# Kernel tuning notes

Measured on AMD Instinct MI355X. Metric: run time of the kernel, lower is better.

## Reference

```python
import jax, jax.numpy as jnp
import numpy as np

B, M, PAST, FUT, NPRED, D = 512, 32768, 8, 12, 20, 48


def _gru_step(h, x, w_ih, w_hh, b_ih, b_hh):
    # torch GRU cell: gates ordered [r, z, n]
    gi = x @ w_ih.T + b_ih
    gh = h @ w_hh.T + b_hh
    ir, iz, inn = jnp.split(gi, 3, axis=-1)
    hr, hz, hn = jnp.split(gh, 3, axis=-1)
    r = jax.nn.sigmoid(ir + hr)
    z = jax.nn.sigmoid(iz + hz)
    n = jnp.tanh(inn + r * hn)
    return (1.0 - z) * n + z * h


def setup_inputs() -> dict:
    key = jax.random.key(0)
    ks = jax.random.split(key, 16)
    f32 = jnp.float32
    def rn(k, shp, sc):
        return (jax.random.normal(k, shp, dtype=f32) * sc)
    return {
        "past": jax.random.normal(ks[0], (B, PAST, 2), dtype=f32),
        "obs_traj": jax.random.normal(ks[1], (B, PAST, 2), dtype=f32),
        "conv_w": rn(ks[2], (D, 2, 3), 0.3),
        "conv_b": jnp.zeros((D,), f32),
        "enc_w_ih": rn(ks[3], (3 * D, D), 0.1),
        "enc_w_hh": rn(ks[4], (3 * D, D), 0.1),
        "enc_b_ih": jnp.zeros((3 * D,), f32),
        "enc_b_hh": jnp.zeros((3 * D,), f32),
        "memory_past": jax.random.normal(ks[5], (M, D), dtype=f32),
        "memory_fut": jax.random.normal(ks[6], (M, D), dtype=f32),
        "Wq": rn(ks[7], (D, D), 0.1), "bq": jnp.zeros((D,), f32),
        "Wk": rn(ks[8], (D, D), 0.1), "bk": jnp.zeros((D,), f32),
        "Wv": rn(ks[9], (D, D), 0.1), "bv": jnp.zeros((D,), f32),
        "dec_w_ih": rn(ks[10], (6 * D, 2 * D), 0.1),
        "dec_w_hh": rn(ks[11], (6 * D, 2 * D), 0.1),
        "dec_b_ih": jnp.zeros((6 * D,), f32),
        "dec_b_hh": jnp.zeros((6 * D,), f32),
        "fc_w": rn(ks[12], (2, 2 * D), 0.1),
        "fc_b": jnp.zeros((2,), f32),
    }


def reference(past, obs_traj, conv_w, conv_b, enc_w_ih, enc_w_hh, enc_b_ih, enc_b_hh,
              memory_past, memory_fut, Wq, bq, Wk, bk, Wv, bv,
              dec_w_ih, dec_w_hh, dec_b_ih, dec_b_hh, fc_w, fc_b):
    b = past.shape[0]
    # --- past encoder: Conv1d(2,48,3,pad=1) + ReLU, then GRU(48,48) ---
    x = jnp.transpose(past, (0, 2, 1))                     # [B,2,T]
    emb = jax.lax.conv_general_dilated(
        x, conv_w, (1,), [(1, 1)], dimension_numbers=("NCH", "OIH", "NCH"))
    emb = jax.nn.relu(emb + conv_b[None, :, None])         # [B,48,T]
    emb = jnp.transpose(emb, (2, 0, 1))                    # [T,B,48] for scan

    def enc_step(h, x_t):
        return _gru_step(h, x_t, enc_w_ih, enc_w_hh, enc_b_ih, enc_b_hh), None
    state_past, _ = jax.lax.scan(enc_step, jnp.zeros((b, D), past.dtype), emb)  # [B,48]

    # --- iterative refinement: 20 rounds of attention over the full memory ---
    # Lin_K/Lin_V are applied to the same (full) banks every iteration -> hoist.
    K = memory_past @ Wk.T + bk                            # [M,48]
    V = memory_fut @ Wv.T + bv                             # [M,48]

    def irm_step(c, _):
        q = c @ Wq.T + bq                                  # [B,48]
        a = jax.nn.softmax(q @ K.T, axis=-1)               # [B,M], scale=1.0
        att = a @ V                                        # [B,48]
        return q + att, att
    _, atts = jax.lax.scan(irm_step, state_past, None, length=NPRED)  # [20,B,48]
    pred = jnp.transpose(atts, (1, 0, 2)).reshape(-1, D)   # [B*20,48] (b-major)

    # --- GRU(96,96) decoder, future_len steps, input only at t=0 ---
    n = b * NPRED
    present = jnp.repeat(obs_traj[:, -1], NPRED, axis=0)   # [B*20,2]
    sp = jnp.repeat(state_past, NPRED, axis=0)             # [B*20,48]
    info = jnp.concatenate([sp, pred], axis=1)             # [B*20,96]
    xs = jnp.concatenate(
        [info[None], jnp.zeros((FUT - 1, n, 2 * D), info.dtype)], axis=0)

    def dec_step(carry, x_t):
        h, pres = carry
        h = _gru_step(h, x_t, dec_w_ih, dec_w_hh, dec_b_ih, dec_b_hh)
        pres = pres + (h @ fc_w.T + fc_b)
        return (h, pres), pres
    _, coords = jax.lax.scan(
        dec_step, (jnp.zeros((n, 2 * D), info.dtype), present), xs)  # [FUT,B*20,2]

    prediction = jnp.transpose(coords, (1, 0, 2)).reshape(b, NPRED, FUT, 2)
    return prediction
```

## Files before the change

kernel.cpp:

```cpp
#include <hip/hip_runtime.h>

typedef unsigned short u16;
typedef unsigned int u32;
typedef __attribute__((ext_vector_type(8))) short short8v;
typedef __attribute__((ext_vector_type(4))) float f32x4;

#define GLD_LDS(g, l) __builtin_amdgcn_global_load_lds( \
    (const __attribute__((address_space(1))) void*)(g), \
    (__attribute__((address_space(3))) void*)(l), 16, 0, 0)

#define LOG2E 1.44269504f

__device__ __forceinline__ u16 f2bf(float f){
  union { float f; u32 u; } v; v.f = f;
  u32 r = v.u + 0x7FFFu + ((v.u >> 16) & 1u);
  return (u16)(r >> 16);
}
__device__ __forceinline__ float bf2f(u16 h){
  union { u32 u; float f; } v; v.u = ((u32)h) << 16;
  return v.f;
}
__device__ __forceinline__ u32 pk2(float a, float b){
  union { float f; u32 u; } x, y; x.f = a; y.f = b;
  return __builtin_amdgcn_perm(y.u + 0x8000u, x.u + 0x8000u, 0x07060302u);
}
__device__ __forceinline__ float sigm(float x){ return 1.f/(1.f+__expf(-x)); }
__device__ __forceinline__ float tanh_fast(float x){ return 1.f - 2.f/(1.f+__expf(2.f*x)); }

__global__ __launch_bounds__(256) void setup_kernel(
    const float* past, const float* conv_w, const float* conv_b,
    const float* enc_w_ih, const float* enc_w_hh, const float* enc_b_ih, const float* enc_b_hh,
    const float* memory_past, const float* memory_fut,
    const float* Wq, const float* bq, const float* Wk, const float* bk,
    const float* Wv, const float* bv,
    const float* dec_w_ih, const float* dec_w_hh,
    float* stateP, float* qf, u16* qbB,
    u16* Kb, u16* Vc, u16* Dihf, u16* Dhhf, u16* WqF)
{
  __shared__ __align__(16) char SMEM[61440];
  const int tid = threadIdx.x, bx = blockIdx.x;
  const int wid = tid>>6, lane = tid&63, qd = lane>>4, ln = lane&15;
  f32x4 zf = {0.f,0.f,0.f,0.f};

  if (tid < 108){
    int which = (tid >= 54) ? 1 : 0;
    int e = bx*54 + (tid - which*54);
    const float* src = which ? dec_w_hh : dec_w_ih;
    u16* dst = which ? Dhhf : Dihf;
    int j = e&7, l2 = (e>>3)&15, q2 = (e>>7)&3, tkc = e>>9;
    int kc = tkc % 3, nt = tkc / 3;
    dst[e] = f2bf(src[(nt*16+l2)*96 + kc*32 + q2*8 + j]);
  }
  if (bx < 12){
    int e = bx*256 + tid;
    int j = e&7, l2 = (e>>3)&15, q2 = (e>>7)&3, tkc = e>>9;
    int kc = tkc&1, nt = tkc>>1;
    int g = nt*16+l2, k = kc*32+q2*8+j;
    WqF[e] = (k < 48) ? f2bf(Wq[g*48+k]) : (u16)0;
  }

  if (bx >= 504){
    int eb = bx - 504;
    u16* sWih = (u16*)(SMEM);
    u16* sWhh = (u16*)(SMEM + 18432);
    u16* sWq  = (u16*)(SMEM + 36864);
    float* sCw = (float*)(SMEM + 43008);
    float* sCb = (float*)(SMEM + 44160);
    float* sPast = (float*)(SMEM + 44352);
    u16* sHbW = (u16*)(SMEM + 48448 + wid*2304);
    for (int e0 = tid; e0 < 21504; e0 += 256){
      int e = e0; const float* src; u16* dst;
      if (e < 9216){ src = enc_w_ih; dst = sWih; }
      else if (e < 18432){ e -= 9216; src = enc_w_hh; dst = sWhh; }
      else { e -= 18432; src = Wq; dst = sWq; }
      int j = e&7, l2 = (e>>3)&15, q2 = (e>>7)&3, tkc = e>>9;
      int kc = tkc&1, nt = tkc>>1;
      int g = nt*16+l2, k = kc*32+q2*8+j;
      dst[e] = (k < 48) ? f2bf(src[g*48+k]) : (u16)0;
    }
    for (int i = tid; i < 288; i += 256) sCw[i] = conv_w[i];
    if (tid < 48) sCb[tid] = conv_b[tid];
    for (int i = tid; i < 1024; i += 256) sPast[i] = past[eb*1024 + i];
    __syncthreads();
    short8v aE[8][2];
    {
      const float* pr = &sPast[(wid*16 + ln)*16];
      for (int t = 0; t < 8; ++t)
        for (int kc = 0; kc < 2; ++kc){
          union { short8v v; u16 h[8]; } u;
          #pragma unroll
          for (int j = 0; j < 8; ++j){
            int d = kc*32 + qd*8 + j;
            float a = 0.f;
            if (d < 48){
              a = sCb[d];
              #pragma unroll
              for (int kt = 0; kt < 3; ++kt){
                int tau = t + kt - 1;
                if (tau >= 0 && tau < 8){
                  a += pr[tau*2+0]*sCw[d*6+kt];
                  a += pr[tau*2+1]*sCw[d*6+3+kt];
                }
              }
              a = fmaxf(a, 0.f);
            }
            u.h[j] = (d < 48) ? f2bf(a) : (u16)0;
          }
          aE[t][kc] = u.v;
        }
    }
    for (int i = lane; i < 576; i += 64) ((u32*)sHbW)[i] = 0;
    float biR[3],biZ[3],biN[3],bhR[3],bhZ[3],bhN[3];
    #pragma unroll
    for (int i = 0; i < 3; ++i){
      int d = i*16 + ln;
      biR[i]=enc_b_ih[d]; biZ[i]=enc_b_ih[48+d]; biN[i]=enc_b_ih[96+d];
      bhR[i]=enc_b_hh[d]; bhZ[i]=enc_b_hh[48+d]; bhN[i]=enc_b_hh[96+d];
    }
    float hreg[3][4];
    #pragma unroll
    for (int i=0;i<3;++i) for (int r=0;r<4;++r) hreg[i][r]=0.f;
    int r0 = eb*64 + wid*16;
    #pragma unroll 1
    for (int t = 0; t < 8; ++t){
      short8v aH0 = *(const short8v*)&sHbW[ln*72 + qd*8];
      short8v aH1 = *(const short8v*)&sHbW[ln*72 + 32 + qd*8];
      f32x4 gI[9], gH[9];
      #pragma unroll
      for (int nt = 0; nt < 9; ++nt){ gI[nt] = zf; gH[nt] = zf; }
      #pragma unroll
      for (int nt = 0; nt < 9; ++nt){
        gI[nt] = __builtin_amdgcn_mfma_f32_16x16x32_bf16(aE[t][0], *(const short8v*)&sWih[((nt*2+0)*4+qd)*128 + ln*8], gI[nt], 0,0,0);
        gI[nt] = __builtin_amdgcn_mfma_f32_16x16x32_bf16(aE[t][1], *(const short8v*)&sWih[((nt*2+1)*4+qd)*128 + ln*8], gI[nt], 0,0,0);
        gH[nt] = __builtin_amdgcn_mfma_f32_16x16x32_bf16(aH0, *(const short8v*)&sWhh[((nt*2+0)*4+qd)*128 + ln*8], gH[nt], 0,0,0);
        gH[nt] = __builtin_amdgcn_mfma_f32_16x16x32_bf16(aH1, *(const short8v*)&sWhh[((nt*2+1)*4+qd)*128 + ln*8], gH[nt], 0,0,0);
      }
      #pragma unroll
      for (int i3 = 0; i3 < 3; ++i3)
        #pragma unroll
        for (int r = 0; r < 4; ++r){
          float rr = sigm(gI[i3][r]+biR[i3] + gH[i3][r]+bhR[i3]);
          float zz = sigm(gI[i3+3][r]+biZ[i3] + gH[i3+3][r]+bhZ[i3]);
          float nn = tanh_fast(gI[i3+6][r]+biN[i3] + rr*(gH[i3+6][r]+bhN[i3]));
          float hv = (1.f-zz)*nn + zz*hreg[i3][r];
          hreg[i3][r] = hv;
          sHbW[(qd*4+r)*72 + i3*16 + ln] = f2bf(hv);
        }
    }
    #pragma unroll
    for (int i3 = 0; i3 < 3; ++i3)
      #pragma unroll
      for (int r = 0; r < 4; ++r)
        stateP[(r0+qd*4+r)*48 + i3*16 + ln] = hreg[i3][r];
    short8v aH0 = *(const short8v*)&sHbW[ln*72 + qd*8];
    short8v aH1 = *(const short8v*)&sHbW[ln*72 + 32 + qd*8];
    f32x4 q3[3];
    #pragma unroll
    for (int nt = 0; nt < 3; ++nt){
      q3[nt] = zf;
      q3[nt] = __builtin_amdgcn_mfma_f32_16x16x32_bf16(aH0, *(const short8v*)&sWq[((nt*2+0)*4+qd)*128 + ln*8], q3[nt], 0,0,0);
      q3[nt] = __builtin_amdgcn_mfma_f32_16x16x32_bf16(aH1, *(const short8v*)&sWq[((nt*2+1)*4+qd)*128 + ln*8], q3[nt], 0,0,0);
    }
    #pragma unroll
    for (int nt = 0; nt < 3; ++nt)
      #pragma unroll
      for (int r = 0; r < 4; ++r){
        int row = r0 + qd*4 + r, d = nt*16 + ln;
        float v = q3[nt][r] + bq[d];
        qf[row*48 + d] = v;
        qbB[row*64 + d] = f2bf(v * LOG2E);
      }
    #pragma unroll
    for (int r = 0; r < 4; ++r)
      if (ln < 8) *(u32*)&qbB[(r0+qd*4+r)*64 + 48 + ln*2] = 0;
  } else {
    u16* sWkF = (u16*)(SMEM);
    u16* sWvF = (u16*)(SMEM + 6144);
    u16* smp  = (u16*)(SMEM + 12288 + wid*2304);
    u16* smf  = (u16*)(SMEM + 21504 + wid*2304);
    for (int e0 = tid; e0 < 6144; e0 += 256){
      int e = e0; const float* src; u16* dst;
      if (e < 3072){ src = Wk; dst = sWkF; } else { e -= 3072; src = Wv; dst = sWvF; }
      int j = e&7, l2 = (e>>3)&15, q2 = (e>>7)&3, tkc = e>>9;
      int kc = tkc&1, nt = tkc>>1;
      int g = nt*16+l2, k = kc*32+q2*8+j;
      dst[e] = (k < 48) ? f2bf(src[g*48+k]) : (u16)0;
    }
    __syncthreads();
    int ntile = (bx < 8) ? 2 : 1;
    for (int tt = 0; tt < ntile; ++tt){
      int tile = (tt == 0) ? bx : (504 + bx);
      int r0 = tile*64 + wid*16;
      for (int i = lane; i < 576; i += 64){ ((u32*)smp)[i] = 0; ((u32*)smf)[i] = 0; }
      for (int i = lane; i < 768; i += 64){
        int r = i/48, c = i - r*48;
        smp[r*72+c] = f2bf(memory_past[(size_t)r0*48 + i]);
        smf[r*72+c] = f2bf(memory_fut[(size_t)r0*48 + i]);
      }
      short8v aP0 = *(const short8v*)&smp[ln*72 + qd*8];
      short8v aP1 = *(const short8v*)&smp[ln*72 + 32 + qd*8];
      short8v aF0 = *(const short8v*)&smf[ln*72 + qd*8];
      short8v aF1 = *(const short8v*)&smf[ln*72 + 32 + qd*8];
      f32x4 k3[3], v3[3];
      #pragma unroll
      for (int nt = 0; nt < 3; ++nt){ k3[nt] = zf; v3[nt] = zf; }
      #pragma unroll
      for (int nt = 0; nt < 3; ++nt){
        k3[nt] = __builtin_amdgcn_mfma_f32_16x16x32_bf16(aP0, *(const short8v*)&sWkF[((nt*2+0)*4+qd)*128 + ln*8], k3[nt], 0,0,0);
        k3[nt] = __builtin_amdgcn_mfma_f32_16x16x32_bf16(aP1, *(const short8v*)&sWkF[((nt*2+1)*4+qd)*128 + ln*8], k3[nt], 0,0,0);
        v3[nt] = __builtin_amdgcn_mfma_f32_16x16x32_bf16(aF0, *(const short8v*)&sWvF[((nt*2+0)*4+qd)*128 + ln*8], v3[nt], 0,0,0);
        v3[nt] = __builtin_amdgcn_mfma_f32_16x16x32_bf16(aF1, *(const short8v*)&sWvF[((nt*2+1)*4+qd)*128 + ln*8], v3[nt], 0,0,0);
      }
      #pragma unroll
      for (int nt = 0; nt < 3; ++nt)
        #pragma unroll
        for (int r = 0; r < 4; ++r){
          int key = r0 + qd*4 + r, d = nt*16 + ln;
          Kb[(size_t)key*64 + d] = f2bf(k3[nt][r] + bk[d]);
          Vc[((size_t)(key>>8)*48 + d)*256 + (key&255)] = f2bf(v3[nt][r] + bv[d]);
        }
      #pragma unroll
      for (int r = 0; r < 4; ++r)
        if (ln < 8){ int key = r0 + qd*4 + r; *(u32*)&Kb[(size_t)key*64 + 48 + ln*2] = 0; }
    }
  }
}

__global__ __launch_bounds__(256) void iter_kernel(int mode, int it,
    const u16* qbB, const u16* Kb, const u16* Vc, const u16* WqF, const float* bq,
    const float* qfP, float* qfC, float* pred,
    const float* mP, const float* lP, const float* aP,
    float* mC, float* lC, float* aC)
{
  __shared__ __align__(16) char SMEM[55936];
  u16*   sQ  = (u16*)(SMEM + 45056);
  float* sWc = (float*)(SMEM + 49152);
  float* sLg = (float*)(SMEM + 51200);
  u16*   sCb = (u16*)(SMEM + 51332);
  const int tid = threadIdx.x, bx = blockIdx.x;
  const int wid = tid>>6, lane = tid&63, qd = lane>>4, ln = lane&15;
  const int rg = bx>>4, ch = bx&15;
  const int rowbase = rg*32;
  f32x4 zf = {0.f,0.f,0.f,0.f};

  const int wslice = ch*2048 + wid*512;
  short8v kf0[4][2], vf0[2][3];
  {
    const u16* kb = Kb + (size_t)wslice*64;
    const u16* vb = Vc + (size_t)(wslice>>8)*48*256 + (wslice & 255);
    #pragma unroll
    for (int nt = 0; nt < 4; ++nt)
      #pragma unroll
      for (int kc = 0; kc < 2; ++kc)
        kf0[nt][kc] = *(const short8v*)&kb[(nt*16+ln)*64 + kc*32 + qd*8];
    #pragma unroll
    for (int kc = 0; kc < 2; ++kc)
      #pragma unroll
      for (int dt = 0; dt < 3; ++dt)
        vf0[kc][dt] = *(const short8v*)&vb[(dt*16+ln)*256 + kc*32 + qd*8];
  }

  if (mode == 1){
    float* sRed = (float*)SMEM;
    {
      int row = tid>>3, jj = tid&7, grow = rowbase + row;
      float m0 = mP[grow*16 + jj*2], m1 = mP[grow*16 + jj*2+1];
      float l0 = lP[grow*16 + jj*2], l1 = lP[grow*16 + jj*2+1];
      float mg = fmaxf(m0, m1);
      #pragma unroll
      for (int k = 1; k < 8; k <<= 1) mg = fmaxf(mg, __shfl_xor(mg, k));
      float w0 = exp2f(m0 - mg), w1 = exp2f(m1 - mg);
      float wl = w0*l0 + w1*l1;
      #pragma unroll
      for (int k = 1; k < 8; k <<= 1) wl += __shfl_xor(wl, k);
      sWc[row*16 + jj*2] = w0; sWc[row*16 + jj*2+1] = w1;
      if (jj == 0) sLg[row] = wl;
    }
    __syncthreads();
    {
      f32x4 accv[6];
      #pragma unroll
      for (int i = 0; i < 6; ++i) accv[i] = zf;
      #pragma unroll
      for (int ci = 0; ci < 4; ++ci){
        int c = wid*4 + ci;
        const f32x4* slab = (const f32x4*)(aP + ((size_t)c*512 + rowbase)*48);
        #pragma unroll
        for (int i = 0; i < 6; ++i){
          f32x4 v = slab[i*64 + lane];
          int rr = (i*64 + lane)/12;
          float w = sWc[rr*16 + c];
          accv[i][0] += w*v[0]; accv[i][1] += w*v[1];
          accv[i][2] += w*v[2]; accv[i][3] += w*v[3];
        }
      }
      float* red = sRed + wid*1536;
      #pragma unroll
      for (int i = 0; i < 6; ++i)
        *(f32x4*)&red[(i*64 + lane)*4] = accv[i];
    }
    __syncthreads();
    {
      int row = tid>>3, jj = tid&7, grow = rowbase + row;
      float lg = sLg[row];
      int base = row*48 + jj*6;
      #pragma unroll
      for (int d6 = 0; d6 < 6; ++d6){
        int d = jj*6 + d6;
        float s = sRed[base+d6] + sRed[1536+base+d6] + sRed[3072+base+d6] + sRed[4608+base+d6];
        float a = s / lg;
        if (ch == 0) pred[(size_t)(grow*20 + (it-1))*48 + d] = a;
        sCb[row*72 + d] = f2bf(qfP[grow*48 + d] + a);
      }
      ((u32*)&sCb[row*72 + 48])[jj] = 0;
    }
    __syncthreads();
    if (wid < 2){
      short8v ac0 = *(const short8v*)&sCb[(wid*16+ln)*72 + qd*8];
      short8v ac1 = *(const short8v*)&sCb[(wid*16+ln)*72 + 32 + qd*8];
      f32x4 q3[3];
      #pragma unroll
      for (int nt = 0; nt < 3; ++nt){
        q3[nt] = zf;
        q3[nt] = __builtin_amdgcn_mfma_f32_16x16x32_bf16(ac0, *(const short8v*)&WqF[((nt*2+0)*4+qd)*128 + ln*8], q3[nt], 0,0,0);
        q3[nt] = __builtin_amdgcn_mfma_f32_16x16x32_bf16(ac1, *(const short8v*)&WqF[((nt*2+1)*4+qd)*128 + ln*8], q3[nt], 0,0,0);
      }
      #pragma unroll
      for (int nt = 0; nt < 3; ++nt)
        #pragma unroll
        for (int r = 0; r < 4; ++r){
          int lr = wid*16 + qd*4 + r, d = nt*16 + ln;
          float v = q3[nt][r] + bq[d];
          if (ch == 0) qfC[(rowbase + lr)*48 + d] = v;
          sQ[lr*64 + d] = f2bf(v * LOG2E);
        }
    } else {
      for (int i = tid-128; i < 256; i += 128){
        int r2 = i>>3, p = i&7;
        ((u32*)&sQ[r2*64 + 48])[p] = 0;
      }
    }
    __syncthreads();
  } else {
    const u32* src = (const u32*)(qbB + rowbase*64);
    ((u32*)sQ)[tid]       = src[tid];
    ((u32*)sQ)[256 + tid] = src[256 + tid];
    ((u32*)sQ)[512 + tid] = src[512 + tid];
    ((u32*)sQ)[768 + tid] = src[768 + tid];
    __syncthreads();
  }

  u16* sp8 = (u16*)(SMEM + 26624);
  short8v aq[2][2];
  #pragma unroll
  for (int rt = 0; rt < 2; ++rt)
    #pragma unroll
    for (int kc = 0; kc < 2; ++kc)
      aq[rt][kc] = *(const short8v*)&sQ[(rt*16+ln)*64 + kc*32 + qd*8];
  f32x4 acc[2][3];
  #pragma unroll
  for (int rt = 0; rt < 2; ++rt) for (int dt = 0; dt < 3; ++dt) acc[rt][dt] = zf;
  float mrun[2] = {-3.0e38f, -3.0e38f}, lrun[2] = {0.f, 0.f};
  u16* spb[2] = { sp8 + (wid*2+0)*1152, sp8 + (wid*2+1)*1152 };

  #pragma unroll
  for (int kt = 0; kt < 8; ++kt){
    const int tb = wslice + kt*64;
    const u16* kb = Kb + (size_t)tb*64;
    const u16* vb = Vc + (size_t)(tb>>8)*48*256 + (tb & 255);
    short8v kf[4][2], vf[2][3];
    if (kt == 0){
      #pragma unroll
      for (int nt = 0; nt < 4; ++nt)
        #pragma unroll
        for (int kc = 0; kc < 2; ++kc) kf[nt][kc] = kf0[nt][kc];
      #pragma unroll
      for (int kc = 0; kc < 2; ++kc)
        #pragma unroll
        for (int dt = 0; dt < 3; ++dt) vf[kc][dt] = vf0[kc][dt];
    } else {
      #pragma unroll
      for (int nt = 0; nt < 4; ++nt)
        #pragma unroll
        for (int kc = 0; kc < 2; ++kc)
          kf[nt][kc] = *(const short8v*)&kb[(nt*16+ln)*64 + kc*32 + qd*8];
      #pragma unroll
      for (int kc = 0; kc < 2; ++kc)
        #pragma unroll
        for (int dt = 0; dt < 3; ++dt)
          vf[kc][dt] = *(const short8v*)&vb[(dt*16+ln)*256 + kc*32 + qd*8];
    }
    f32x4 s[2][4];
    #pragma unroll
    for (int rt = 0; rt < 2; ++rt)
      #pragma unroll
      for (int nt = 0; nt < 4; ++nt){
        f32x4 z = zf;
        z = __builtin_amdgcn_mfma_f32_16x16x32_bf16(kf[nt][0], aq[rt][0], z, 0,0,0);
        z = __builtin_amdgcn_mfma_f32_16x16x32_bf16(kf[nt][1], aq[rt][1], z, 0,0,0);
        s[rt][nt] = z;
      }
    #pragma unroll
    for (int rt = 0; rt < 2; ++rt){
      float vmax = fmaxf(fmaxf(fmaxf(s[rt][0][0], s[rt][0][1]), fmaxf(s[rt][0][2], s[rt][0][3])),
                   fmaxf(fmaxf(s[rt][1][0], s[rt][1][1]), fmaxf(s[rt][1][2], s[rt][1][3])));
      vmax = fmaxf(vmax, fmaxf(fmaxf(fmaxf(s[rt][2][0], s[rt][2][1]), fmaxf(s[rt][2][2], s[rt][2][3])),
                   fmaxf(fmaxf(s[rt][3][0], s[rt][3][1]), fmaxf(s[rt][3][2], s[rt][3][3]))));
      vmax = fmaxf(vmax, __shfl_xor(vmax, 16));
      vmax = fmaxf(vmax, __shfl_xor(vmax, 32));
      float mnew = fmaxf(mrun[rt], vmax);
      float alpha = exp2f(mrun[rt] - mnew);
      mrun[rt] = mnew;
      u16* sp = spb[rt];
      float lsum = 0.f;
      #pragma unroll
      for (int nt = 0; nt < 4; ++nt){
        float p0 = exp2f(s[rt][nt][0]-mnew), p1 = exp2f(s[rt][nt][1]-mnew);
        float p2 = exp2f(s[rt][nt][2]-mnew), p3 = exp2f(s[rt][nt][3]-mnew);
        lsum += (p0+p1)+(p2+p3);
        uint2 pk; pk.x = pk2(p0,p1); pk.y = pk2(p2,p3);
        *(uint2*)&sp[ln*72 + nt*16 + qd*4] = pk;
      }
      lsum += __shfl_xor(lsum, 16);
      lsum += __shfl_xor(lsum, 32);
      lrun[rt] = lrun[rt]*alpha + lsum;
      #pragma unroll
      for (int dt = 0; dt < 3; ++dt){
        acc[rt][dt][0] *= alpha; acc[rt][dt][1] *= alpha;
        acc[rt][dt][2] *= alpha; acc[rt][dt][3] *= alpha;
      }
      short8v pb0 = *(const short8v*)&sp[ln*72 + qd*8];
      short8v pb1 = *(const short8v*)&sp[ln*72 + 32 + qd*8];
      #pragma unroll
      for (int dt = 0; dt < 3; ++dt){
        acc[rt][dt] = __builtin_amdgcn_mfma_f32_16x16x32_bf16(vf[0][dt], pb0, acc[rt][dt], 0,0,0);
        acc[rt][dt] = __builtin_amdgcn_mfma_f32_16x16x32_bf16(vf[1][dt], pb1, acc[rt][dt], 0,0,0);
      }
    }
  }
  __syncthreads();
  float* sMg = (float*)SMEM;
  #pragma unroll
  for (int rt = 0; rt < 2; ++rt)
    #pragma unroll
    for (int dt = 0; dt < 3; ++dt)
      #pragma unroll
      for (int r = 0; r < 4; ++r)
        sMg[wid*1600 + (rt*16+ln)*50 + dt*16 + qd*4 + r] = acc[rt][dt][r];
  if (lane < 16){
    sMg[wid*1600 + ln*50 + 48] = mrun[0]; sMg[wid*1600 + ln*50 + 49] = lrun[0];
    sMg[wid*1600 + (16+ln)*50 + 48] = mrun[1]; sMg[wid*1600 + (16+ln)*50 + 49] = lrun[1];
  }
  __syncthreads();
  {
    int row = tid>>3, jj = tid&7, grow = rowbase + row;
    float m0 = sMg[row*50+48], m1 = sMg[1600+row*50+48];
    float m2 = sMg[3200+row*50+48], m3 = sMg[4800+row*50+48];
    float mg = fmaxf(fmaxf(m0,m1), fmaxf(m2,m3));
    float e0 = exp2f(m0-mg), e1 = exp2f(m1-mg), e2 = exp2f(m2-mg), e3 = exp2f(m3-mg);
    float lg = e0*sMg[row*50+49] + e1*sMg[1600+row*50+49]
             + e2*sMg[3200+row*50+49] + e3*sMg[4800+row*50+49];
    if (jj == 0){ mC[grow*16 + ch] = mg; lC[grow*16 + ch] = lg; }
    int d0 = jj*6;
    #pragma unroll
    for (int d6 = 0; d6 < 6; ++d6){
      int d = d0 + d6;
      aC[((size_t)ch*512 + grow)*48 + d] =
          e0*sMg[row*50+d] + e1*sMg[1600+row*50+d]
        + e2*sMg[3200+row*50+d] + e3*sMg[4800+row*50+d];
    }
  }
}

__global__ __launch_bounds__(64) void dec_kernel(
    const u16* Dihf, const u16* Dhhf, const float* b_ih, const float* b_hh,
    const float* stateP, const float* pred, const float* obs,
    const float* mF, const float* lF, const float* aF,
    const float* fc_w, const float* fc_b, float* out)
{
  __shared__ __align__(16) u16 sW[27648];
  __shared__ __align__(16) u16 sx[16*104];
  const int lane = threadIdx.x, bx = blockIdx.x;
  const int qd = lane>>4, ln = lane&15;
  f32x4 zf = {0.f,0.f,0.f,0.f};
  const int rw = bx*16;

  #pragma unroll 1
  for (int i = 0; i < 54; ++i)
    GLD_LDS((const char*)Dhhf + i*1024 + lane*16, (char*)sW + i*1024);

  for (int i = lane; i < 1536; i += 64){
    int r = i/96, k = i - r*96;
    int row = rw + r, b20 = row/20;
    float v = (k < 48) ? stateP[b20*48 + k] : pred[(size_t)row*48 + (k-48)];
    sx[r*104 + k] = f2bf(v);
  }
  {
    int r19 = (19 - (rw % 20)) % 20;
    if (r19 < 16 && lane < 48){
      int b = (rw + r19)/20;
      float mg = -3.0e38f;
      float mv[16];
      #pragma unroll
      for (int c = 0; c < 16; ++c){ mv[c] = mF[b*16 + c]; mg = fmaxf(mg, mv[c]); }
      float num = 0.f, den = 0.f;
      #pragma unroll
      for (int c = 0; c < 16; ++c){
        float w = exp2f(mv[c] - mg);
        den += w * lF[b*16 + c];
        num += w * aF[((size_t)c*512 + b)*48 + lane];
      }
      sx[r19*104 + 48 + lane] = f2bf(num/den);
    }
  }
  __syncthreads();

  float fw0[6], fw1[6];
  float biR[6],biZ[6],biN[6],bhR[6],bhZ[6],bhN[6];
  #pragma unroll
  for (int i = 0; i < 6; ++i){
    int d = i*16 + ln;
    fw0[i] = fc_w[d]; fw1[i] = fc_w[96+d];
    biR[i]=b_ih[d]; biZ[i]=b_ih[96+d]; biN[i]=b_ih[192+d];
    bhR[i]=b_hh[d]; bhZ[i]=b_hh[96+d]; bhN[i]=b_hh[192+d];
  }
  float fcb0 = fc_b[0], fcb1 = fc_b[1];
  float pr0[4], pr1[4];
  #pragma unroll
  for (int r = 0; r < 4; ++r){
    int b20 = (rw + qd*4 + r)/20;
    pr0[r] = obs[b20*16 + 14];
    pr1[r] = obs[b20*16 + 15];
  }

  {
    short8v xa0 = *(const short8v*)&sx[ln*104 + qd*8];
    short8v xa1 = *(const short8v*)&sx[ln*104 + 32 + qd*8];
    short8v xa2 = *(const short8v*)&sx[ln*104 + 64 + qd*8];
    f32x4 acc[18];
    #pragma unroll
    for (int i = 0; i < 18; ++i) acc[i] = zf;
    #pragma unroll
    for (int nt = 0; nt < 18; ++nt){
      acc[nt] = __builtin_amdgcn_mfma_f32_16x16x32_bf16(xa0, *(const short8v*)&Dihf[((nt*3+0)*4+qd)*128 + ln*8], acc[nt], 0,0,0);
      acc[nt] = __builtin_amdgcn_mfma_f32_16x16x32_bf16(xa1, *(const short8v*)&Dihf[((nt*3+1)*4+qd)*128 + ln*8], acc[nt], 0,0,0);
      acc[nt] = __builtin_amdgcn_mfma_f32_16x16x32_bf16(xa2, *(const short8v*)&Dihf[((nt*3+2)*4+qd)*128 + ln*8], acc[nt], 0,0,0);
    }
    float px[4] = {0,0,0,0}, py[4] = {0,0,0,0};
    #pragma unroll
    for (int r = 0; r < 4; ++r)
      #pragma unroll
      for (int i = 0; i < 6; ++i){
        int d = i*16 + ln;
        float rr = sigm(acc[i][r]   + biR[i] + bhR[i]);
        float zz = sigm(acc[i+6][r] + biZ[i] + bhZ[i]);
        float nn = tanh_fast(acc[i+12][r] + biN[i] + rr*bhN[i]);
        float hv = (1.f-zz)*nn;
        sx[(qd*4+r)*104 + d] = f2bf(hv);
        px[r] += fw0[i]*hv;
        py[r] += fw1[i]*hv;
      }
    #pragma unroll
    for (int msk = 8; msk >= 1; msk >>= 1)
      #pragma unroll
      for (int r = 0; r < 4; ++r){
        px[r] += __shfl_xor(px[r], msk);
        py[r] += __shfl_xor(py[r], msk);
      }
    #pragma unroll
    for (int r = 0; r < 4; ++r){
      pr0[r] += px[r] + fcb0;
      pr1[r] += py[r] + fcb1;
    }
    if (ln == 0){
      #pragma unroll
      for (int r = 0; r < 4; ++r){
        int row = rw + qd*4 + r;
        out[(size_t)(row*12 + 0)*2 + 0] = pr0[r];
        out[(size_t)(row*12 + 0)*2 + 1] = pr1[r];
      }
    }
  }
  __syncthreads();

  #pragma unroll 1
  for (int t = 1; t < 12; ++t){
    short8v xa0 = *(const short8v*)&sx[ln*104 + qd*8];
    short8v xa1 = *(const short8v*)&sx[ln*104 + 32 + qd*8];
    short8v xa2 = *(const short8v*)&sx[ln*104 + 64 + qd*8];
    f32x4 acc[18];
    #pragma unroll
    for (int i = 0; i < 18; ++i) acc[i] = zf;
    #pragma unroll
    for (int nt = 0; nt < 18; ++nt){
      acc[nt] = __builtin_amdgcn_mfma_f32_16x16x32_bf16(xa0, *(const short8v*)&sW[((nt*3+0)*4+qd)*128 + ln*8], acc[nt], 0,0,0);
      acc[nt] = __builtin_amdgcn_mfma_f32_16x16x32_bf16(xa1, *(const short8v*)&sW[((nt*3+1)*4+qd)*128 + ln*8], acc[nt], 0,0,0);
      acc[nt] = __builtin_amdgcn_mfma_f32_16x16x32_bf16(xa2, *(const short8v*)&sW[((nt*3+2)*4+qd)*128 + ln*8], acc[nt], 0,0,0);
    }
    float px[4] = {0,0,0,0}, py[4] = {0,0,0,0};
    #pragma unroll
    for (int r = 0; r < 4; ++r)
      #pragma unroll
      for (int i = 0; i < 6; ++i){
        int d = i*16 + ln;
        float rr = sigm(acc[i][r]   + biR[i] + bhR[i]);
        float zz = sigm(acc[i+6][r] + biZ[i] + bhZ[i]);
        float nn = tanh_fast(biN[i] + rr*(acc[i+12][r] + bhN[i]));
        float hold = bf2f(sx[(qd*4+r)*104 + d]);
        float hv = (1.f-zz)*nn + zz*hold;
        sx[(qd*4+r)*104 + d] = f2bf(hv);
        px[r] += fw0[i]*hv;
        py[r] += fw1[i]*hv;
      }
    #pragma unroll
    for (int msk = 8; msk >= 1; msk >>= 1)
      #pragma unroll
      for (int r = 0; r < 4; ++r){
        px[r] += __shfl_xor(px[r], msk);
        py[r] += __shfl_xor(py[r], msk);
      }
    #pragma unroll
    for (int r = 0; r < 4; ++r){
      pr0[r] += px[r] + fcb0;
      pr1[r] += py[r] + fcb1;
    }
    if (ln == 0){
      #pragma unroll
      for (int r = 0; r < 4; ++r){
        int row = rw + qd*4 + r;
        out[(size_t)(row*12 + t)*2 + 0] = pr0[r];
        out[(size_t)(row*12 + t)*2 + 1] = pr1[r];
      }
    }
  }
}

extern "C" void kernel_launch(void* const* d_in, const int* in_sizes, int n_in,
                              void* d_out, int out_size, void* d_ws, size_t ws_size,
                              hipStream_t stream)
{
  const float* past        = (const float*)d_in[0];
  const float* obs         = (const float*)d_in[1];
  const float* conv_w      = (const float*)d_in[2];
  const float* conv_b      = (const float*)d_in[3];
  const float* enc_w_ih    = (const float*)d_in[4];
  const float* enc_w_hh    = (const float*)d_in[5];
  const float* enc_b_ih    = (const float*)d_in[6];
  const float* enc_b_hh    = (const float*)d_in[7];
  const float* memory_past = (const float*)d_in[8];
  const float* memory_fut  = (const float*)d_in[9];
  const float* Wq = (const float*)d_in[10];
  const float* bq = (const float*)d_in[11];
  const float* Wk = (const float*)d_in[12];
  const float* bk = (const float*)d_in[13];
  const float* Wv = (const float*)d_in[14];
  const float* bv = (const float*)d_in[15];
  const float* dec_w_ih = (const float*)d_in[16];
  const float* dec_w_hh = (const float*)d_in[17];
  const float* dec_b_ih = (const float*)d_in[18];
  const float* dec_b_hh = (const float*)d_in[19];
  const float* fc_w = (const float*)d_in[20];
  const float* fc_b = (const float*)d_in[21];
  float* out = (float*)d_out;

  char* ws = (char*)d_ws;
  size_t off = 0;
  auto alloc = [&](size_t bytes){ void* p = ws + off; off += (bytes + 255) & ~(size_t)255; return p; };
  float* stateP = (float*)alloc(512*48*4);
  float* qfA    = (float*)alloc(512*48*4);
  float* qfB    = (float*)alloc(512*48*4);
  u16*   qbB    = (u16*)alloc(512*64*2);
  float* mB[2], *lB[2], *aB[2];
  for (int i = 0; i < 2; ++i){
    mB[i] = (float*)alloc(512*16*4);
    lB[i] = (float*)alloc(512*16*4);
    aB[i] = (float*)alloc((size_t)512*16*48*4);
  }
  float* pred = (float*)alloc((size_t)10240*48*4);
  u16*   Kb   = (u16*)alloc((size_t)32768*64*2);
  u16*   Vc   = (u16*)alloc((size_t)32768*48*2);
  u16*   Dihf = (u16*)alloc(27648*2);
  u16*   Dhhf = (u16*)alloc(27648*2);
  u16*   WqF  = (u16*)alloc(3072*2);
  float* qbuf[2] = { qfA, qfB };

  setup_kernel<<<512, 256, 0, stream>>>(
      past, conv_w, conv_b, enc_w_ih, enc_w_hh, enc_b_ih, enc_b_hh,
      memory_past, memory_fut, Wq, bq, Wk, bk, Wv, bv, dec_w_ih, dec_w_hh,
      stateP, qfA, qbB, Kb, Vc, Dihf, Dhhf, WqF);

  iter_kernel<<<256, 256, 0, stream>>>(0, 0, qbB, Kb, Vc, WqF, bq,
      qfA, qfA, pred, mB[1], lB[1], aB[1], mB[0], lB[0], aB[0]);
  for (int it = 1; it < 20; ++it){
    int pv = (it-1)&1, cu = it&1;
    iter_kernel<<<256, 256, 0, stream>>>(1, it, qbB, Kb, Vc, WqF, bq,
        qbuf[pv], qbuf[cu], pred, mB[pv], lB[pv], aB[pv], mB[cu], lB[cu], aB[cu]);
  }

  dec_kernel<<<640, 64, 0, stream>>>(Dihf, Dhhf, dec_b_ih, dec_b_hh,
      stateP, pred, obs, mB[1], lB[1], aB[1], fc_w, fc_b, out);
}
```

Measured before the change: 719.0 us.

## Split decoder GRU across three waves with register-resident W_hh, drop K/V prefetch

The decoder kernel goes from one wave per 16-row block to three waves. Each wave owns a third of the hidden units and holds its slice of the recurrent weights in registers instead of staging the full W_hh into LDS. Hidden state is double-buffered in LDS, and the fc partial sums are reduced across waves through shared memory, at the cost of one barrier per step. Separately, the iter_kernel no longer prefetches the first K/V tile before the mode-dependent prologue, which frees registers but loses that load overlap.

```diff
diff --git a/kernel.cpp b/kernel.cpp
--- a/kernel.cpp
+++ b/kernel.cpp
@@ -4,10 +4,6 @@
 typedef unsigned int u32;
 typedef __attribute__((ext_vector_type(8))) short short8v;
 typedef __attribute__((ext_vector_type(4))) float f32x4;
-
-#define GLD_LDS(g, l) __builtin_amdgcn_global_load_lds( \
-    (const __attribute__((address_space(1))) void*)(g), \
-    (__attribute__((address_space(3))) void*)(l), 16, 0, 0)
 
 #define LOG2E 1.44269504f
 
@@ -243,23 +239,6 @@
   const int rowbase = rg*32;
   f32x4 zf = {0.f,0.f,0.f,0.f};
 
-  const int wslice = ch*2048 + wid*512;
-  short8v kf0[4][2], vf0[2][3];
-  {
-    const u16* kb = Kb + (size_t)wslice*64;
-    const u16* vb = Vc + (size_t)(wslice>>8)*48*256 + (wslice & 255);
-    #pragma unroll
-    for (int nt = 0; nt < 4; ++nt)
-      #pragma unroll
-      for (int kc = 0; kc < 2; ++kc)
-        kf0[nt][kc] = *(const short8v*)&kb[(nt*16+ln)*64 + kc*32 + qd*8];
-    #pragma unroll
-    for (int kc = 0; kc < 2; ++kc)
-      #pragma unroll
-      for (int dt = 0; dt < 3; ++dt)
-        vf0[kc][dt] = *(const short8v*)&vb[(dt*16+ln)*256 + kc*32 + qd*8];
-  }
-
   if (mode == 1){
     float* sRed = (float*)SMEM;
     {
@@ -350,6 +329,7 @@
     __syncthreads();
   }
 
+  const int wslice = ch*2048 + wid*512;
   u16* sp8 = (u16*)(SMEM + 26624);
   short8v aq[2][2];
   #pragma unroll
@@ -369,27 +349,16 @@
     const u16* kb = Kb + (size_t)tb*64;
     const u16* vb = Vc + (size_t)(tb>>8)*48*256 + (tb & 255);
     short8v kf[4][2], vf[2][3];
-    if (kt == 0){
-      #pragma unroll
-      for (int nt = 0; nt < 4; ++nt)
-        #pragma unroll
-        for (int kc = 0; kc < 2; ++kc) kf[nt][kc] = kf0[nt][kc];
+    #pragma unroll
+    for (int nt = 0; nt < 4; ++nt)
       #pragma unroll
       for (int kc = 0; kc < 2; ++kc)
-        #pragma unroll
-        for (int dt = 0; dt < 3; ++dt) vf[kc][dt] = vf0[kc][dt];
-    } else {
-      #pragma unroll
-      for (int nt = 0; nt < 4; ++nt)
-        #pragma unroll
-        for (int kc = 0; kc < 2; ++kc)
-          kf[nt][kc] = *(const short8v*)&kb[(nt*16+ln)*64 + kc*32 + qd*8];
-      #pragma unroll
-      for (int kc = 0; kc < 2; ++kc)
-        #pragma unroll
-        for (int dt = 0; dt < 3; ++dt)
-          vf[kc][dt] = *(const short8v*)&vb[(dt*16+ln)*256 + kc*32 + qd*8];
-    }
+        kf[nt][kc] = *(const short8v*)&kb[(nt*16+ln)*64 + kc*32 + qd*8];
+    #pragma unroll
+    for (int kc = 0; kc < 2; ++kc)
+      #pragma unroll
+      for (int dt = 0; dt < 3; ++dt)
+        vf[kc][dt] = *(const short8v*)&vb[(dt*16+ln)*256 + kc*32 + qd*8];
     f32x4 s[2][4];
     #pragma unroll
     for (int rt = 0; rt < 2; ++rt)
@@ -472,35 +441,30 @@
   }
 }
 
-__global__ __launch_bounds__(64) void dec_kernel(
+__global__ __launch_bounds__(192) void dec_kernel(
     const u16* Dihf, const u16* Dhhf, const float* b_ih, const float* b_hh,
     const float* stateP, const float* pred, const float* obs,
     const float* mF, const float* lF, const float* aF,
     const float* fc_w, const float* fc_b, float* out)
 {
-  __shared__ __align__(16) u16 sW[27648];
-  __shared__ __align__(16) u16 sx[16*104];
-  const int lane = threadIdx.x, bx = blockIdx.x;
-  const int qd = lane>>4, ln = lane&15;
+  __shared__ __align__(16) u16 sx[2][16*104];
+  __shared__ float sPx[2][3][16], sPy[2][3][16];
+  const int tid = threadIdx.x, bx = blockIdx.x;
+  const int wid = tid/64, lane = tid%64, qd = (lane>>4), ln = lane&15;
+  const int rw = bx*16;
   f32x4 zf = {0.f,0.f,0.f,0.f};
-  const int rw = bx*16;
-
-  #pragma unroll 1
-  for (int i = 0; i < 54; ++i)
-    GLD_LDS((const char*)Dhhf + i*1024 + lane*16, (char*)sW + i*1024);
-
-  for (int i = lane; i < 1536; i += 64){
+
+  for (int i = tid; i < 1536; i += 192){
     int r = i/96, k = i - r*96;
     int row = rw + r, b20 = row/20;
     float v = (k < 48) ? stateP[b20*48 + k] : pred[(size_t)row*48 + (k-48)];
-    sx[r*104 + k] = f2bf(v);
-  }
-  {
+    sx[0][r*104 + k] = f2bf(v);
+  }
+  if (tid < 48){
     int r19 = (19 - (rw % 20)) % 20;
-    if (r19 < 16 && lane < 48){
+    if (r19 < 16){
       int b = (rw + r19)/20;
-      float mg = -3.0e38f;
-      float mv[16];
+      float mg = -3.0e38f, mv[16];
       #pragma unroll
       for (int c = 0; c < 16; ++c){ mv[c] = mF[b*16 + c]; mg = fmaxf(mg, mv[c]); }
       float num = 0.f, den = 0.f;
@@ -508,57 +472,81 @@
       for (int c = 0; c < 16; ++c){
         float w = exp2f(mv[c] - mg);
         den += w * lF[b*16 + c];
-        num += w * aF[((size_t)c*512 + b)*48 + lane];
-      }
-      sx[r19*104 + 48 + lane] = f2bf(num/den);
-    }
+        num += w * aF[((size_t)c*512 + b)*48 + tid];
+      }
+      sx[0][r19*104 + 48 + tid] = f2bf(num/den);
+    }
+  }
+  short8v whh[6][3];
+  #pragma unroll
+  for (int g = 0; g < 3; ++g)
+    #pragma unroll
+    for (int u = 0; u < 2; ++u){
+      int nt = g*6 + wid*2 + u;
+      #pragma unroll
+      for (int kc = 0; kc < 3; ++kc)
+        whh[g*2+u][kc] = *(const short8v*)&Dhhf[((nt*3+kc)*4+qd)*128 + ln*8];
+    }
+  float biR[2],biZ[2],biN[2],bhR[2],bhZ[2],bhN[2],fw0[2],fw1[2];
+  #pragma unroll
+  for (int u = 0; u < 2; ++u){
+    int d = (wid*2+u)*16 + ln;
+    biR[u]=b_ih[d]; biZ[u]=b_ih[96+d]; biN[u]=b_ih[192+d];
+    bhR[u]=b_hh[d]; bhZ[u]=b_hh[96+d]; bhN[u]=b_hh[192+d];
+    fw0[u]=fc_w[d]; fw1[u]=fc_w[96+d];
+  }
+  float hold[2][4];
+  #pragma unroll
+  for (int u = 0; u < 2; ++u) for (int r = 0; r < 4; ++r) hold[u][r] = 0.f;
+  float fcb0 = fc_b[0], fcb1 = fc_b[1];
+  float pres0 = 0.f, pres1 = 0.f;
+  if (wid == 0 && lane < 16){
+    int b20 = (rw + lane)/20;
+    pres0 = obs[b20*16 + 14];
+    pres1 = obs[b20*16 + 15];
   }
   __syncthreads();
 
-  float fw0[6], fw1[6];
-  float biR[6],biZ[6],biN[6],bhR[6],bhZ[6],bhN[6];
-  #pragma unroll
-  for (int i = 0; i < 6; ++i){
-    int d = i*16 + ln;
-    fw0[i] = fc_w[d]; fw1[i] = fc_w[96+d];
-    biR[i]=b_ih[d]; biZ[i]=b_ih[96+d]; biN[i]=b_ih[192+d];
-    bhR[i]=b_hh[d]; bhZ[i]=b_hh[96+d]; bhN[i]=b_hh[192+d];
-  }
-  float fcb0 = fc_b[0], fcb1 = fc_b[1];
-  float pr0[4], pr1[4];
-  #pragma unroll
-  for (int r = 0; r < 4; ++r){
-    int b20 = (rw + qd*4 + r)/20;
-    pr0[r] = obs[b20*16 + 14];
-    pr1[r] = obs[b20*16 + 15];
-  }
-
-  {
-    short8v xa0 = *(const short8v*)&sx[ln*104 + qd*8];
-    short8v xa1 = *(const short8v*)&sx[ln*104 + 32 + qd*8];
-    short8v xa2 = *(const short8v*)&sx[ln*104 + 64 + qd*8];
-    f32x4 acc[18];
-    #pragma unroll
-    for (int i = 0; i < 18; ++i) acc[i] = zf;
-    #pragma unroll
-    for (int nt = 0; nt < 18; ++nt){
-      acc[nt] = __builtin_amdgcn_mfma_f32_16x16x32_bf16(xa0, *(const short8v*)&Dihf[((nt*3+0)*4+qd)*128 + ln*8], acc[nt], 0,0,0);
-      acc[nt] = __builtin_amdgcn_mfma_f32_16x16x32_bf16(xa1, *(const short8v*)&Dihf[((nt*3+1)*4+qd)*128 + ln*8], acc[nt], 0,0,0);
-      acc[nt] = __builtin_amdgcn_mfma_f32_16x16x32_bf16(xa2, *(const short8v*)&Dihf[((nt*3+2)*4+qd)*128 + ln*8], acc[nt], 0,0,0);
+  #pragma unroll 1
+  for (int t = 0; t < 12; ++t){
+    const u16* sr = sx[t&1];
+    u16* sw = sx[(t+1)&1];
+    short8v xa0 = *(const short8v*)&sr[ln*104 + qd*8];
+    short8v xa1 = *(const short8v*)&sr[ln*104 + 32 + qd*8];
+    short8v xa2 = *(const short8v*)&sr[ln*104 + 64 + qd*8];
+    f32x4 acc[6];
+    #pragma unroll
+    for (int i = 0; i < 6; ++i) acc[i] = zf;
+    if (t == 0){
+      #pragma unroll
+      for (int j6 = 0; j6 < 6; ++j6){
+        int nt = (j6>>1)*6 + wid*2 + (j6&1);
+        acc[j6] = __builtin_amdgcn_mfma_f32_16x16x32_bf16(xa0, *(const short8v*)&Dihf[((nt*3+0)*4+qd)*128 + ln*8], acc[j6], 0,0,0);
+        acc[j6] = __builtin_amdgcn_mfma_f32_16x16x32_bf16(xa1, *(const short8v*)&Dihf[((nt*3+1)*4+qd)*128 + ln*8], acc[j6], 0,0,0);
+        acc[j6] = __builtin_amdgcn_mfma_f32_16x16x32_bf16(xa2, *(const short8v*)&Dihf[((nt*3+2)*4+qd)*128 + ln*8], acc[j6], 0,0,0);
+      }
+    } else {
+      #pragma unroll
+      for (int j6 = 0; j6 < 6; ++j6){
+        acc[j6] = __builtin_amdgcn_mfma_f32_16x16x32_bf16(xa0, whh[j6][0], acc[j6], 0,0,0);
+        acc[j6] = __builtin_amdgcn_mfma_f32_16x16x32_bf16(xa1, whh[j6][1], acc[j6], 0,0,0);
+        acc[j6] = __builtin_amdgcn_mfma_f32_16x16x32_bf16(xa2, whh[j6][2], acc[j6], 0,0,0);
+      }
     }
     float px[4] = {0,0,0,0}, py[4] = {0,0,0,0};
     #pragma unroll
     for (int r = 0; r < 4; ++r)
       #pragma unroll
-      for (int i = 0; i < 6; ++i){
-        int d = i*16 + ln;
-        float rr = sigm(acc[i][r]   + biR[i] + bhR[i]);
-        float zz = sigm(acc[i+6][r] + biZ[i] + bhZ[i]);
-        float nn = tanh_fast(acc[i+12][r] + biN[i] + rr*bhN[i]);
-        float hv = (1.f-zz)*nn;
-        sx[(qd*4+r)*104 + d] = f2bf(hv);
-        px[r] += fw0[i]*hv;
-        py[r] += fw1[i]*hv;
+      for (int u = 0; u < 2; ++u){
+        float rr = sigm(acc[0+u][r] + biR[u] + bhR[u]);
+        float zz = sigm(acc[2+u][r] + biZ[u] + bhZ[u]);
+        float nn = (t == 0) ? tanh_fast(acc[4+u][r] + biN[u] + rr*bhN[u])
+                            : tanh_fast(biN[u] + rr*(acc[4+u][r] + bhN[u]));
+        float hv = (1.f-zz)*nn + zz*hold[u][r];
+        hold[u][r] = hv;
+        sw[(qd*4+r)*104 + (wid*2+u)*16 + ln] = f2bf(hv);
+        px[r] += fw0[u]*hv;
+        py[r] += fw1[u]*hv;
       }
     #pragma unroll
     for (int msk = 8; msk >= 1; msk >>= 1)
@@ -567,70 +555,21 @@
         px[r] += __shfl_xor(px[r], msk);
         py[r] += __shfl_xor(py[r], msk);
       }
-    #pragma unroll
-    for (int r = 0; r < 4; ++r){
-      pr0[r] += px[r] + fcb0;
-      pr1[r] += py[r] + fcb1;
-    }
     if (ln == 0){
       #pragma unroll
       for (int r = 0; r < 4; ++r){
-        int row = rw + qd*4 + r;
-        out[(size_t)(row*12 + 0)*2 + 0] = pr0[r];
-        out[(size_t)(row*12 + 0)*2 + 1] = pr1[r];
-      }
-    }
-  }
-  __syncthreads();
-
-  #pragma unroll 1
-  for (int t = 1; t < 12; ++t){
-    short8v xa0 = *(const short8v*)&sx[ln*104 + qd*8];
-    short8v xa1 = *(const short8v*)&sx[ln*104 + 32 + qd*8];
-    short8v xa2 = *(const short8v*)&sx[ln*104 + 64 + qd*8];
-    f32x4 acc[18];
-    #pragma unroll
-    for (int i = 0; i < 18; ++i) acc[i] = zf;
-    #pragma unroll
-    for (int nt = 0; nt < 18; ++nt){
-      acc[nt] = __builtin_amdgcn_mfma_f32_16x16x32_bf16(xa0, *(const short8v*)&sW[((nt*3+0)*4+qd)*128 + ln*8], acc[nt], 0,0,0);
-      acc[nt] = __builtin_amdgcn_mfma_f32_16x16x32_bf16(xa1, *(const short8v*)&sW[((nt*3+1)*4+qd)*128 + ln*8], acc[nt], 0,0,0);
-      acc[nt] = __builtin_amdgcn_mfma_f32_16x16x32_bf16(xa2, *(const short8v*)&sW[((nt*3+2)*4+qd)*128 + ln*8], acc[nt], 0,0,0);
-    }
-    float px[4] = {0,0,0,0}, py[4] = {0,0,0,0};
-    #pragma unroll
-    for (int r = 0; r < 4; ++r)
-      #pragma unroll
-      for (int i = 0; i < 6; ++i){
-        int d = i*16 + ln;
-        float rr = sigm(acc[i][r]   + biR[i] + bhR[i]);
-        float zz = sigm(acc[i+6][r] + biZ[i] + bhZ[i]);
-        float nn = tanh_fast(biN[i] + rr*(acc[i+12][r] + bhN[i]));
-        float hold = bf2f(sx[(qd*4+r)*104 + d]);
-        float hv = (1.f-zz)*nn + zz*hold;
-        sx[(qd*4+r)*104 + d] = f2bf(hv);
-        px[r] += fw0[i]*hv;
-        py[r] += fw1[i]*hv;
-      }
-    #pragma unroll
-    for (int msk = 8; msk >= 1; msk >>= 1)
-      #pragma unroll
-      for (int r = 0; r < 4; ++r){
-        px[r] += __shfl_xor(px[r], msk);
-        py[r] += __shfl_xor(py[r], msk);
-      }
-    #pragma unroll
-    for (int r = 0; r < 4; ++r){
-      pr0[r] += px[r] + fcb0;
-      pr1[r] += py[r] + fcb1;
-    }
-    if (ln == 0){
-      #pragma unroll
-      for (int r = 0; r < 4; ++r){
-        int row = rw + qd*4 + r;
-        out[(size_t)(row*12 + t)*2 + 0] = pr0[r];
-        out[(size_t)(row*12 + t)*2 + 1] = pr1[r];
-      }
+        sPx[t&1][wid][qd*4+r] = px[r];
+        sPy[t&1][wid][qd*4+r] = py[r];
+      }
+    }
+    __syncthreads();
+    if (wid == 0 && lane < 16){
+      float fx = sPx[t&1][0][lane] + sPx[t&1][1][lane] + sPx[t&1][2][lane];
+      float fy = sPy[t&1][0][lane] + sPy[t&1][1][lane] + sPy[t&1][2][lane];
+      pres0 += fx + fcb0;
+      pres1 += fy + fcb1;
+      out[((size_t)(rw + lane)*12 + t)*2 + 0] = pres0;
+      out[((size_t)(rw + lane)*12 + t)*2 + 1] = pres1;
     }
   }
 }
@@ -697,6 +636,6 @@
         qbuf[pv], qbuf[cu], pred, mB[pv], lB[pv], aB[pv], mB[cu], lB[cu], aB[cu]);
   }
 
-  dec_kernel<<<640, 64, 0, stream>>>(Dihf, Dhhf, dec_b_ih, dec_b_hh,
+  dec_kernel<<<640, 192, 0, stream>>>(Dihf, Dhhf, dec_b_ih, dec_b_hh,
       stateP, pred, obs, mB[1], lB[1], aB[1], fc_w, fc_b, out);
 }
```

New measurement: 644.3 us. -10.4%, faster.
